# Kernel optimization log

Hardware: AMD Instinct MI355X
Metric: run time of the kernel (lower is better)

Reference implementation:

```python
import jax, jax.numpy as jnp
import numpy as np

NH = 16  # matches init kwarg nh


def setup_inputs() -> dict:
    key = jax.random.key(0)
    k1, k2 = jax.random.split(key)
    b, S, T = 4, 4096, 4096
    x = jax.random.normal(k1, (b, S, 1), dtype=jnp.float32)
    coords_rel = jax.random.normal(k2, (2, b, S, T), dtype=jnp.float32)
    return {"x": x, "coords_rel": coords_rel}


def reference(x, coords_rel):
    # coords_rel: [2, b, S, T]; x: [b, S, 1]
    d = jnp.sqrt(coords_rel[0] ** 2 + coords_rel[1] ** 2)            # [b, S, T]
    # torch.topk(d, NH, dim=1, largest=False): smallest NH along source dim, ascending
    neg_vals, idx = jax.lax.top_k(jnp.transpose(-d, (0, 2, 1)), NH)  # [b, T, NH]
    dist_abs = jnp.transpose(-neg_vals, (0, 2, 1))                   # [b, NH, T]
    indices = jnp.transpose(idx, (0, 2, 1))                          # [b, NH, T]
    b, nh, t = dist_abs.shape
    w = 1.0 / (dist_abs + 1e-15) ** 2                                # [b, nh, t]
    denom = w.sum(axis=2)                                            # [b, nh] (sum over t, as in source)
    # faithful reproduction of torch .view(t,b,nh) raw reinterpretation + broadcast divide + .view(b,t,nh)
    w = (w.reshape(t, b, nh) / denom).reshape(b, t, nh)              # [b, t, nh]
    S = x.shape[1]
    idx_btn = indices.reshape(b, t, nh)                              # raw reshape, matches torch .view
    # gather: out[i,j,k] = x[i, idx[i,j,k], 0]  (x.repeat over last dim makes all columns equal)
    xg = jnp.take_along_axis(jnp.broadcast_to(x, (b, S, nh)), idx_btn, axis=1)  # [b, t, nh]
    out = (xg * w).sum(axis=2)                                       # [b, t]
    return out[..., None]                                            # [b, t, 1]
```

## Files before the change

### kernel.cpp

```cpp
#include <hip/hip_runtime.h>

#define B_ 4
#define S_ 4096
#define T_ 4096
#define NH_ 16
#define CPB 32
#define CPW 2
#define ROWS 64
#define NTILE (S_ / ROWS)
#define LDSP 33
#define NCG (T_ / CPB)

typedef unsigned long long u64;

__device__ __forceinline__ float dpp_shr1_f(float v) {
    return __int_as_float(__builtin_amdgcn_update_dpp(
        0, __float_as_int(v), 0x111 , 0xF, 0xF, true));
}
__device__ __forceinline__ int dpp_shr1_i(int v) {
    return __builtin_amdgcn_update_dpp(0, v, 0x111, 0xF, 0xF, true);
}

__global__ __launch_bounds__(1024, 8) void topk_scan(
    const float* __restrict__ coords,
    float* __restrict__ outW,
    int*   __restrict__ outI,
    float* __restrict__ partials)
{
    __shared__ float lds[2][ROWS * LDSP];
    __shared__ float red[16 * NH_];

    const int bid  = blockIdx.x;
    const int b    = bid >> 7;
    const int c0   = (bid & (NCG - 1)) * CPB;
    const int tid  = threadIdx.x;
    const int w    = tid >> 6;
    const int lane = tid & 63;

    const size_t plane = (size_t)B_ * S_ * T_;
    const bool stager = (tid < 512);
    const int  srow = tid >> 3;
    const int  scol = (tid & 7) * 4;
    const float* g0 = coords + (size_t)b * S_ * T_ + (size_t)srow * T_ + (c0 + scol);
    const float* g1 = g0 + plane;
    float* wb0 = &lds[0][srow * LDSP + scol];
    float* wb1 = &lds[1][srow * LDSP + scol];

    float lv[CPW]; int li[CPW]; float tau[CPW];
#pragma unroll
    for (int cc = 0; cc < CPW; ++cc) {
        lv[cc]  = __int_as_float(0x7f800000);
        li[cc]  = 0;
        tau[cc] = __int_as_float(0x7f800000);
    }

    float4 ax, ay;
    if (stager) {
        ax = *(const float4*)g0;  ay = *(const float4*)g1;
        wb0[0] = __fadd_rn(__fmul_rn(ax.x, ax.x), __fmul_rn(ay.x, ay.x));
        wb0[1] = __fadd_rn(__fmul_rn(ax.y, ax.y), __fmul_rn(ay.y, ay.y));
        wb0[2] = __fadd_rn(__fmul_rn(ax.z, ax.z), __fmul_rn(ay.z, ay.z));
        wb0[3] = __fadd_rn(__fmul_rn(ax.w, ax.w), __fmul_rn(ay.w, ay.w));
        ax = *(const float4*)(g0 + (size_t)ROWS * T_);
        ay = *(const float4*)(g1 + (size_t)ROWS * T_);
    }
    __syncthreads();

#pragma unroll 1
    for (int k = 0; k < NTILE; ++k) {
        if (stager) {
            if (k + 1 < NTILE) {
                float* wb = (k & 1) ? wb0 : wb1;
                wb[0] = __fadd_rn(__fmul_rn(ax.x, ax.x), __fmul_rn(ay.x, ay.x));
                wb[1] = __fadd_rn(__fmul_rn(ax.y, ax.y), __fmul_rn(ay.y, ay.y));
                wb[2] = __fadd_rn(__fmul_rn(ax.z, ax.z), __fmul_rn(ay.z, ay.z));
                wb[3] = __fadd_rn(__fmul_rn(ax.w, ax.w), __fmul_rn(ay.w, ay.w));
            }
            if (k + 2 < NTILE) {
                ax = *(const float4*)(g0 + (size_t)(k + 2) * ROWS * T_);
                ay = *(const float4*)(g1 + (size_t)(k + 2) * ROWS * T_);
            }
        }

        const float* rb = lds[k & 1];
        if (k == 0) {
#pragma unroll
            for (int cc = 0; cc < CPW; ++cc) {
                const float d2 = rb[lane * LDSP + (w * CPW + cc)];
                u64 key = ((u64)(unsigned)__float_as_int(d2) << 32) | (unsigned)lane;
#pragma unroll
                for (int bk = 2; bk <= 64; bk <<= 1) {
#pragma unroll
                    for (int bj = bk >> 1; bj > 0; bj >>= 1) {
                        const u64 o = __shfl_xor(key, bj);
                        const bool takemin = ((lane & bj) == 0) == ((lane & bk) == 0);
                        key = ((key < o) == takemin) ? key : o;
                    }
                }
                lv[cc]  = __int_as_float((int)(unsigned)(key >> 32));
                li[cc]  = (int)(key & 0xFFFFFFFFu);
                tau[cc] = __int_as_float(
                    __builtin_amdgcn_readlane(__float_as_int(lv[cc]), NH_ - 1));
            }
        } else {
#pragma unroll
            for (int cc = 0; cc < CPW; ++cc) {
                const float d2 = rb[lane * LDSP + (w * CPW + cc)];
                u64 m = __ballot(d2 < tau[cc]);
                if (m) {
                    while (m) {
                        const int src = __ffsll(m) - 1;
                        m &= m - 1;
                        const float cd = __int_as_float(
                            __builtin_amdgcn_readlane(__float_as_int(d2), src));
                        const int   ci = k * ROWS + src;
                        const unsigned pm = (unsigned)__ballot(lv[cc] <= cd) & 0xFFFFu;
                        const int p = __popc(pm);
                        const float uv = dpp_shr1_f(lv[cc]);
                        const int   ui = dpp_shr1_i(li[cc]);
                        const bool here  = (lane == p);
                        const bool shift = (lane > p) && (lane < NH_);
                        lv[cc] = here ? cd : (shift ? uv : lv[cc]);
                        li[cc] = here ? ci : (shift ? ui : li[cc]);
                    }
                    tau[cc] = __int_as_float(
                        __builtin_amdgcn_readlane(__float_as_int(lv[cc]), NH_ - 1));
                }
            }
        }
        __syncthreads();
    }

    float dsum = 0.f;
#pragma unroll
    for (int cc = 0; cc < CPW; ++cc) {
        const int t = c0 + w * CPW + cc;
        if (lane < NH_) {
            const float d = sqrtf(lv[cc]) + 1e-15f;
            const float wv = 1.0f / (d * d);
            outW[((size_t)b * T_ + t) * NH_ + lane] = wv;
            outI[((size_t)b * T_ + t) * NH_ + lane] = li[cc];
            dsum += wv;
        }
    }
    if (lane < NH_) red[w * NH_ + lane] = dsum;
    __syncthreads();
    if (tid < NH_) {
        float s = 0.f;
#pragma unroll
        for (int q = 0; q < 16; ++q) s += red[q * NH_ + tid];
        partials[(size_t)bid * NH_ + tid] = s;
    }
}

__global__ __launch_bounds__(128) void denom_reduce(
    const float* __restrict__ partials, float* __restrict__ denom)
{
    const int q = blockIdx.x;
    const int b = q >> 4, j = q & 15;
    const int g = threadIdx.x;
    __shared__ float sm[128];
    sm[g] = partials[(size_t)(b * NCG + g) * NH_ + j];
    __syncthreads();
    for (int s = 64; s > 0; s >>= 1) {
        if (g < s) sm[g] += sm[g + s];
        __syncthreads();
    }
    if (g == 0) denom[q] = sm[0];
}

__global__ __launch_bounds__(256) void out_kernel(
    const float* __restrict__ x,
    const float* __restrict__ outW,
    const int*   __restrict__ outI,
    const float* __restrict__ denom,
    float* __restrict__ out)
{
    const int gid16 = blockIdx.x * 256 + threadIdx.x;
    const int oid = gid16 >> 4;
    const int q   = gid16 & 15;
    const int i = oid >> 12;
    const int j = oid & 4095;
    const int ih = j >> 8;
    const size_t base = ((size_t)i * T_ + (size_t)(j & 255) * NH_) * NH_ + ih;
    const float w  = outW[base + (size_t)q * NH_];
    const int   id = outI[base + (size_t)q * NH_];
    float v = x[i * S_ + id] * w / denom[(j & 3) * NH_ + q];
    v += __shfl_xor(v, 1);
    v += __shfl_xor(v, 2);
    v += __shfl_xor(v, 4);
    v += __shfl_xor(v, 8);
    if (q == 0) out[oid] = v;
}

extern "C" void kernel_launch(void* const* d_in, const int* in_sizes, int n_in,
                              void* d_out, int out_size, void* d_ws, size_t ws_size,
                              hipStream_t stream) {
    const float* x      = (const float*)d_in[0];
    const float* coords = (const float*)d_in[1];
    float* out = (float*)d_out;

    float* outW     = (float*)d_ws;
    int*   outI     = (int*)(outW + (size_t)B_ * T_ * NH_);
    float* partials = (float*)(outI + (size_t)B_ * T_ * NH_);
    float* denom    = partials + (size_t)(B_ * NCG) * NH_;

    topk_scan   <<<B_ * NCG,           1024, 0, stream>>>(coords, outW, outI, partials);
    denom_reduce<<<64,                 128,  0, stream>>>(partials, denom);
    out_kernel  <<<B_ * T_ * 16 / 256, 256,  0, stream>>>(x, outW, outI, denom, out);
}
```

Before: 125.9 us.

## Stage two row tiles per phase using all threads to halve block barriers

All 1024 threads now stage coordinates instead of only half, with each half loading one of two 64-row tiles per phase into a doubled LDS buffer. The scan then processes two tiles between barriers, halving the number of __syncthreads and doubling the loads in flight per phase. The cost is double the LDS footprint, which may reduce blocks per CU, and more registers held live across the unrolled inner tile loop.

```diff
diff --git a/kernel.cpp b/kernel.cpp
--- a/kernel.cpp
+++ b/kernel.cpp
@@ -8,6 +8,8 @@
 #define CPW 2
 #define ROWS 64
 #define NTILE (S_ / ROWS)
+#define TPB 2
+#define NPH (NTILE / TPB)
 #define LDSP 33
 #define NCG (T_ / CPB)
 
@@ -19,6 +21,9 @@
 }
 __device__ __forceinline__ int dpp_shr1_i(int v) {
     return __builtin_amdgcn_update_dpp(0, v, 0x111, 0xF, 0xF, true);
+}
+__device__ __forceinline__ float d2_rn(float x, float y) {
+    return __fadd_rn(__fmul_rn(x, x), __fmul_rn(y, y));
 }
 
 __global__ __launch_bounds__(1024, 8) void topk_scan(
@@ -27,7 +32,7 @@
     int*   __restrict__ outI,
     float* __restrict__ partials)
 {
-    __shared__ float lds[2][ROWS * LDSP];
+    __shared__ float lds[2][TPB][ROWS * LDSP];
     __shared__ float red[16 * NH_];
 
     const int bid  = blockIdx.x;
@@ -38,13 +43,13 @@
     const int lane = tid & 63;
 
     const size_t plane = (size_t)B_ * S_ * T_;
-    const bool stager = (tid < 512);
-    const int  srow = tid >> 3;
-    const int  scol = (tid & 7) * 4;
+    const int sub  = tid >> 9;
+    const int srow = (tid >> 3) & 63;
+    const int scol = (tid & 7) * 4;
     const float* g0 = coords + (size_t)b * S_ * T_ + (size_t)srow * T_ + (c0 + scol);
     const float* g1 = g0 + plane;
-    float* wb0 = &lds[0][srow * LDSP + scol];
-    float* wb1 = &lds[1][srow * LDSP + scol];
+    float* wb0 = &lds[0][sub][srow * LDSP + scol];
+    float* wb1 = &lds[1][sub][srow * LDSP + scol];
 
     float lv[CPW]; int li[CPW]; float tau[CPW];
 #pragma unroll
@@ -54,77 +59,73 @@
         tau[cc] = __int_as_float(0x7f800000);
     }
 
-    float4 ax, ay;
-    if (stager) {
-        ax = *(const float4*)g0;  ay = *(const float4*)g1;
-        wb0[0] = __fadd_rn(__fmul_rn(ax.x, ax.x), __fmul_rn(ay.x, ay.x));
-        wb0[1] = __fadd_rn(__fmul_rn(ax.y, ax.y), __fmul_rn(ay.y, ay.y));
-        wb0[2] = __fadd_rn(__fmul_rn(ax.z, ax.z), __fmul_rn(ay.z, ay.z));
-        wb0[3] = __fadd_rn(__fmul_rn(ax.w, ax.w), __fmul_rn(ay.w, ay.w));
-        ax = *(const float4*)(g0 + (size_t)ROWS * T_);
-        ay = *(const float4*)(g1 + (size_t)ROWS * T_);
-    }
+    float4 ax = *(const float4*)(g0 + (size_t)sub * ROWS * T_);
+    float4 ay = *(const float4*)(g1 + (size_t)sub * ROWS * T_);
+    wb0[0] = d2_rn(ax.x, ay.x); wb0[1] = d2_rn(ax.y, ay.y);
+    wb0[2] = d2_rn(ax.z, ay.z); wb0[3] = d2_rn(ax.w, ay.w);
+    ax = *(const float4*)(g0 + (size_t)(TPB + sub) * ROWS * T_);
+    ay = *(const float4*)(g1 + (size_t)(TPB + sub) * ROWS * T_);
     __syncthreads();
 
 #pragma unroll 1
-    for (int k = 0; k < NTILE; ++k) {
-        if (stager) {
-            if (k + 1 < NTILE) {
-                float* wb = (k & 1) ? wb0 : wb1;
-                wb[0] = __fadd_rn(__fmul_rn(ax.x, ax.x), __fmul_rn(ay.x, ay.x));
-                wb[1] = __fadd_rn(__fmul_rn(ax.y, ax.y), __fmul_rn(ay.y, ay.y));
-                wb[2] = __fadd_rn(__fmul_rn(ax.z, ax.z), __fmul_rn(ay.z, ay.z));
-                wb[3] = __fadd_rn(__fmul_rn(ax.w, ax.w), __fmul_rn(ay.w, ay.w));
-            }
-            if (k + 2 < NTILE) {
-                ax = *(const float4*)(g0 + (size_t)(k + 2) * ROWS * T_);
-                ay = *(const float4*)(g1 + (size_t)(k + 2) * ROWS * T_);
-            }
-        }
-
-        const float* rb = lds[k & 1];
-        if (k == 0) {
-#pragma unroll
-            for (int cc = 0; cc < CPW; ++cc) {
-                const float d2 = rb[lane * LDSP + (w * CPW + cc)];
-                u64 key = ((u64)(unsigned)__float_as_int(d2) << 32) | (unsigned)lane;
-#pragma unroll
-                for (int bk = 2; bk <= 64; bk <<= 1) {
-#pragma unroll
-                    for (int bj = bk >> 1; bj > 0; bj >>= 1) {
-                        const u64 o = __shfl_xor(key, bj);
-                        const bool takemin = ((lane & bj) == 0) == ((lane & bk) == 0);
-                        key = ((key < o) == takemin) ? key : o;
+    for (int p = 0; p < NPH; ++p) {
+        if (p + 1 < NPH) {
+            float* wb = (p & 1) ? wb0 : wb1;
+            wb[0] = d2_rn(ax.x, ay.x); wb[1] = d2_rn(ax.y, ay.y);
+            wb[2] = d2_rn(ax.z, ay.z); wb[3] = d2_rn(ax.w, ay.w);
+        }
+        if (p + 2 < NPH) {
+            ax = *(const float4*)(g0 + (size_t)(TPB * (p + 2) + sub) * ROWS * T_);
+            ay = *(const float4*)(g1 + (size_t)(TPB * (p + 2) + sub) * ROWS * T_);
+        }
+
+#pragma unroll
+        for (int s2 = 0; s2 < TPB; ++s2) {
+            const int k = TPB * p + s2;
+            const float* rb = lds[p & 1][s2];
+            if (k == 0) {
+#pragma unroll
+                for (int cc = 0; cc < CPW; ++cc) {
+                    const float d2 = rb[lane * LDSP + (w * CPW + cc)];
+                    u64 key = ((u64)(unsigned)__float_as_int(d2) << 32) | (unsigned)lane;
+#pragma unroll
+                    for (int bk = 2; bk <= 64; bk <<= 1) {
+#pragma unroll
+                        for (int bj = bk >> 1; bj > 0; bj >>= 1) {
+                            const u64 o = __shfl_xor(key, bj);
+                            const bool takemin = ((lane & bj) == 0) == ((lane & bk) == 0);
+                            key = ((key < o) == takemin) ? key : o;
+                        }
                     }
-                }
-                lv[cc]  = __int_as_float((int)(unsigned)(key >> 32));
-                li[cc]  = (int)(key & 0xFFFFFFFFu);
-                tau[cc] = __int_as_float(
-                    __builtin_amdgcn_readlane(__float_as_int(lv[cc]), NH_ - 1));
-            }
-        } else {
-#pragma unroll
-            for (int cc = 0; cc < CPW; ++cc) {
-                const float d2 = rb[lane * LDSP + (w * CPW + cc)];
-                u64 m = __ballot(d2 < tau[cc]);
-                if (m) {
-                    while (m) {
-                        const int src = __ffsll(m) - 1;
-                        m &= m - 1;
-                        const float cd = __int_as_float(
-                            __builtin_amdgcn_readlane(__float_as_int(d2), src));
-                        const int   ci = k * ROWS + src;
-                        const unsigned pm = (unsigned)__ballot(lv[cc] <= cd) & 0xFFFFu;
-                        const int p = __popc(pm);
-                        const float uv = dpp_shr1_f(lv[cc]);
-                        const int   ui = dpp_shr1_i(li[cc]);
-                        const bool here  = (lane == p);
-                        const bool shift = (lane > p) && (lane < NH_);
-                        lv[cc] = here ? cd : (shift ? uv : lv[cc]);
-                        li[cc] = here ? ci : (shift ? ui : li[cc]);
-                    }
+                    lv[cc]  = __int_as_float((int)(unsigned)(key >> 32));
+                    li[cc]  = (int)(key & 0xFFFFFFFFu);
                     tau[cc] = __int_as_float(
                         __builtin_amdgcn_readlane(__float_as_int(lv[cc]), NH_ - 1));
+                }
+            } else {
+#pragma unroll
+                for (int cc = 0; cc < CPW; ++cc) {
+                    const float d2 = rb[lane * LDSP + (w * CPW + cc)];
+                    u64 m = __ballot(d2 < tau[cc]);
+                    if (m) {
+                        while (m) {
+                            const int src = __ffsll(m) - 1;
+                            m &= m - 1;
+                            const float cd = __int_as_float(
+                                __builtin_amdgcn_readlane(__float_as_int(d2), src));
+                            const int   ci = k * ROWS + src;
+                            const unsigned pm = (unsigned)__ballot(lv[cc] <= cd) & 0xFFFFu;
+                            const int p2 = __popc(pm);
+                            const float uv = dpp_shr1_f(lv[cc]);
+                            const int   ui = dpp_shr1_i(li[cc]);
+                            const bool here  = (lane == p2);
+                            const bool shift = (lane > p2) && (lane < NH_);
+                            lv[cc] = here ? cd : (shift ? uv : lv[cc]);
+                            li[cc] = here ? ci : (shift ? ui : li[cc]);
+                        }
+                        tau[cc] = __int_as_float(
+                            __builtin_amdgcn_readlane(__float_as_int(lv[cc]), NH_ - 1));
+                    }
                 }
             }
         }
```

Result: no change. 126.4 us (+0.4%).
